# Kernel tuning notes

Measured on AMD Instinct MI355X. Metric: run time of the kernel, lower is better.

Reference implementation:

```python
import jax, jax.numpy as jnp
import numpy as np

INF = 100000.0
B, W, T, U, S, N = 64, 16, 64, 128, 20, 8


def setup_inputs() -> dict:
    key = jax.random.key(0)
    ks = jax.random.split(key, 9)
    xavier = (2.0 / (U + U)) ** 0.5
    return {
        "slot_utt_h": jax.random.normal(ks[0], (B, W, T, U), jnp.float32),
        "slot_candidate_c": jax.random.normal(ks[1], (S, U), jnp.float32),
        "status_candidate_c": jax.random.normal(ks[2], (N, U), jnp.float32),
        "position_encoding": jax.random.normal(ks[3], (B, W, S, U), jnp.float32),
        "q_status": jax.random.normal(ks[4], (B, W, N, U), jnp.float32),
        "mask": jnp.zeros((B, W, S * N), jnp.float32),
        "weight": jax.random.normal(ks[5], (U, U), jnp.float32) * xavier,  # bilinear co-attention weight [U,U]
        "W1": jax.random.normal(ks[6], (2 * U, U), jnp.float32) * 0.05,
        "b1": jnp.zeros((U,), jnp.float32),
        "W2": jax.random.normal(ks[7], (U, U), jnp.float32) * 0.05,
        "b2": jnp.zeros((U,), jnp.float32),
        "W3": jax.random.normal(ks[8], (U, 1), jnp.float32) * 0.05,
        "b3": jnp.zeros((1,), jnp.float32),
    }


def _zero_mask(p):
    # original: -(p == 0).float() * INF, added before softmax
    return jnp.where(p == 0.0, -INF, 0.0)


def reference(slot_utt_h, slot_candidate_c, status_candidate_c, position_encoding,
              q_status, mask, weight, W1, b1, W2, b2, W3, b3):
    # ---- attention over utterance tokens ----
    # p[b,w,s,t] = <slot_candidate_c[s], slot_utt_h[b,w,t]>
    p = jnp.einsum('su,bwtu->bwst', slot_candidate_c, slot_utt_h)
    p = jax.nn.softmax(p + _zero_mask(p), axis=-1)
    q_slot = jnp.einsum('bwst,bwtu->bwsu', p, slot_utt_h) + position_encoding  # [B,W,S,U]

    # ---- bilinear co-attention: [B,W*S,U] @ weight @ [B,U,W*N] -> [B,W,S,W,N] ----
    co = jnp.einsum('bwsu,uv,bxnv->bwsxn', q_slot, weight, q_status)
    p2 = jax.nn.softmax(co + _zero_mask(co), axis=3)  # softmax over the second window axis x

    # weighted sum of statuses over window axis x
    q_status_slot = jnp.einsum('bwsxn,bxnu->bwsnu', p2, q_status)  # [B,W,S,N,U]

    q_slot_exp = jnp.broadcast_to(q_slot[:, :, :, None, :], (B, W, S, N, U))
    features = jnp.concatenate([q_slot_exp, q_status_slot], axis=-1)  # [B,W,S,N,2U]

    # ---- MLP (dropout in eval mode = identity) ----
    h = jax.nn.relu(features @ W1 + b1)
    h = jax.nn.relu(h @ W2 + b2)
    logits = h @ W3 + b3  # [B,W,S,N,1]

    logits = logits.reshape(B, W, S * N)
    slot_pred_logits = jnp.max(logits + mask, axis=1)  # masked max-pool over window
    slot_pred_labels = (slot_pred_logits > 0.0).astype(jnp.float32)
    return (slot_pred_labels, S * N, slot_pred_logits)
```

## Files before the change

### kernel.cpp

```cpp
#include <hip/hip_runtime.h>
#include <math.h>

#define INF_ 100000.0f
constexpr int B_ = 64, W_ = 16, T_ = 64, U_ = 128, S_ = 20, N_ = 8;

typedef unsigned short ushort_t;
typedef __attribute__((ext_vector_type(8))) short bf16x8;
typedef __attribute__((ext_vector_type(4))) float floatx4;

static __device__ __forceinline__ unsigned short f2bf(float x) {
    unsigned int u = __float_as_uint(x);
    return (unsigned short)((u + 0x7fff + ((u >> 16) & 1)) >> 16);
}
static __device__ __forceinline__ float bf2f(unsigned short s) {
    return __uint_as_float(((unsigned int)s) << 16);
}

__global__ __launch_bounds__(256) void k0_cast(
    const float* __restrict__ q_status, const float* __restrict__ weight,
    const float* __restrict__ W1, const float* __restrict__ W2,
    const float* __restrict__ c,
    ushort_t* __restrict__ qstat_bf, ushort_t* __restrict__ w1topT,
    ushort_t* __restrict__ w1botT, ushort_t* __restrict__ w2T,
    ushort_t* __restrict__ c_bf, ushort_t* __restrict__ Gt_bf)
{
    __shared__ __align__(16) ushort_t sw[128 * 136];
    __shared__ __align__(16) ushort_t sq[128 * 136];

    const int tid = threadIdx.x;

    if (blockIdx.x < 1076) {
        int g = blockIdx.x * 256 + tid;
        if (g < 262144) {
            int i = g * 4;
            float4 v = *(const float4*)&q_status[i];
            ushort4 o = {f2bf(v.x), f2bf(v.y), f2bf(v.z), f2bf(v.w)};
            *(ushort4*)&qstat_bf[i] = o;
            return;
        }
        g -= 262144;
        if (g < 4096) {
            int i = g * 4, j = i >> 7, k = i & 127;
            ushort4 o = {f2bf(W1[k * 128 + j]), f2bf(W1[(k + 1) * 128 + j]),
                         f2bf(W1[(k + 2) * 128 + j]), f2bf(W1[(k + 3) * 128 + j])};
            *(ushort4*)&w1topT[i] = o;
            return;
        }
        g -= 4096;
        if (g < 4096) {
            int i = g * 4, j = i >> 7, k = i & 127;
            ushort4 o = {f2bf(W1[(128 + k) * 128 + j]), f2bf(W1[(129 + k) * 128 + j]),
                         f2bf(W1[(130 + k) * 128 + j]), f2bf(W1[(131 + k) * 128 + j])};
            *(ushort4*)&w1botT[i] = o;
            return;
        }
        g -= 4096;
        if (g < 4096) {
            int i = g * 4, j = i >> 7, k = i & 127;
            ushort4 o = {f2bf(W2[k * 128 + j]), f2bf(W2[(k + 1) * 128 + j]),
                         f2bf(W2[(k + 2) * 128 + j]), f2bf(W2[(k + 3) * 128 + j])};
            *(ushort4*)&w2T[i] = o;
            return;
        }
        g -= 4096;
        if (g < 1024) {
            int i = g * 4, s = i >> 7;
            ushort4 o = {0, 0, 0, 0};
            if (s < 20) {
                float4 v = *(const float4*)&c[i];
                o = (ushort4){f2bf(v.x), f2bf(v.y), f2bf(v.z), f2bf(v.w)};
            }
            *(ushort4*)&c_bf[i] = o;
            return;
        }
        return;
    }

    const int b = blockIdx.x - 1076;
    const float* qb = q_status + (size_t)b * 16384;
    for (int i = tid * 4; i < 16384; i += 1024) {
        int r = i >> 7, v = i & 127;
        float4 wv = *(const float4*)&weight[i];
        ushort4 ow = {f2bf(wv.x), f2bf(wv.y), f2bf(wv.z), f2bf(wv.w)};
        *(ushort4*)&sw[r * 136 + v] = ow;
        float4 qv = *(const float4*)&qb[i];
        ushort4 oq = {f2bf(qv.x), f2bf(qv.y), f2bf(qv.z), f2bf(qv.w)};
        *(ushort4*)&sq[r * 136 + v] = oq;
    }
    __syncthreads();

    const int wave = tid >> 6, lane = tid & 63, m16 = lane & 15, q = lane >> 4;
    ushort_t* Gb = Gt_bf + (size_t)b * 16384;
#pragma unroll
    for (int ci = 0; ci < 16; ++ci) {
        int tile = wave * 16 + ci;
        int mt = tile >> 3, jt = tile & 7;
        floatx4 acc = {0.f, 0.f, 0.f, 0.f};
#pragma unroll
        for (int kt = 0; kt < 4; ++kt) {
            bf16x8 a = *(const bf16x8*)&sq[(mt * 16 + m16) * 136 + kt * 32 + q * 8];
            bf16x8 w = *(const bf16x8*)&sw[(jt * 16 + m16) * 136 + kt * 32 + q * 8];
            acc = __builtin_amdgcn_mfma_f32_16x16x32_bf16(a, w, acc, 0, 0, 0);
        }
#pragma unroll
        for (int reg = 0; reg < 4; ++reg)
            Gb[(mt * 16 + q * 4 + reg) * 128 + jt * 16 + m16] = f2bf(acc[reg]);
    }
}

__global__ __launch_bounds__(256) void k1_attn(
    const float* __restrict__ h,
    const ushort_t* __restrict__ c_bf,
    const float* __restrict__ pos,
    ushort_t* __restrict__ q_slot_bf)
{
    __shared__ __align__(16) ushort_t sh_h[64 * 136];
    __shared__ __align__(16) ushort_t sh_hT[128 * 72];
    __shared__ __align__(16) float    sh_sc[32 * 68];
    __shared__ __align__(16) ushort_t sh_P[32 * 72];

    const int bw = blockIdx.x, tid = threadIdx.x;
    const float* hb = h + (size_t)bw * 8192;
    for (int i = tid; i < 8192; i += 256) {
        int t = i >> 7, u = i & 127;
        ushort_t v = f2bf(hb[i]);
        sh_h[t * 136 + u] = v;
        sh_hT[u * 72 + t] = v;
    }
    for (int i = tid; i < 32 * 72; i += 256) sh_P[i] = 0;
    __syncthreads();

    const int wave = tid >> 6, lane = tid & 63, m16 = lane & 15, q = lane >> 4;

#pragma unroll
    for (int ci = 0; ci < 2; ++ci) {
        int cmb = wave * 2 + ci;
        int mt = cmb >> 2, jt = cmb & 3;
        floatx4 acc = {0.f, 0.f, 0.f, 0.f};
#pragma unroll
        for (int kt = 0; kt < 4; ++kt) {
            bf16x8 a = *(const bf16x8*)&c_bf[(mt * 16 + m16) * 128 + kt * 32 + q * 8];
            bf16x8 b = *(const bf16x8*)&sh_h[(jt * 16 + m16) * 136 + kt * 32 + q * 8];
            acc = __builtin_amdgcn_mfma_f32_16x16x32_bf16(a, b, acc, 0, 0, 0);
        }
#pragma unroll
        for (int reg = 0; reg < 4; ++reg)
            sh_sc[(mt * 16 + q * 4 + reg) * 68 + jt * 16 + m16] = acc[reg];
    }
    __syncthreads();

    for (int s = wave; s < 20; s += 4) {
        float v = sh_sc[s * 68 + lane];
        if (v == 0.0f) v = -INF_;
        float m = v;
        for (int d = 32; d; d >>= 1) m = fmaxf(m, __shfl_xor(m, d));
        float e = expf(v - m);
        float sum = e;
        for (int d = 32; d; d >>= 1) sum += __shfl_xor(sum, d);
        sh_P[s * 72 + lane] = f2bf(e / sum);
    }
    __syncthreads();

    const size_t obase = (size_t)bw * 2560;
#pragma unroll
    for (int ci = 0; ci < 4; ++ci) {
        int cmb = wave * 4 + ci;
        int mt = cmb >> 3, jt = cmb & 7;
        floatx4 acc = {0.f, 0.f, 0.f, 0.f};
#pragma unroll
        for (int kt = 0; kt < 2; ++kt) {
            bf16x8 a = *(const bf16x8*)&sh_P[(mt * 16 + m16) * 72 + kt * 32 + q * 8];
            bf16x8 b = *(const bf16x8*)&sh_hT[(jt * 16 + m16) * 72 + kt * 32 + q * 8];
            acc = __builtin_amdgcn_mfma_f32_16x16x32_bf16(a, b, acc, 0, 0, 0);
        }
        int u = jt * 16 + m16;
#pragma unroll
        for (int reg = 0; reg < 4; ++reg) {
            int row = mt * 16 + q * 4 + reg;
            if (row < 20)
                q_slot_bf[obase + row * 128 + u] =
                    f2bf(acc[reg] + pos[obase + row * 128 + u]);
        }
    }
}

__global__ __launch_bounds__(512, 2) void k2ab(
    const ushort_t* __restrict__ qs_bf,
    const ushort_t* __restrict__ w1topT,
    const float* __restrict__ b1,
    const ushort_t* __restrict__ qstat_bf,
    const ushort_t* __restrict__ w1botT,
    float* __restrict__ A,
    ushort_t* __restrict__ qs1T_bf)
{
    __shared__ __align__(16) ushort_t sh_w[128 * 136];
    const int tid = threadIdx.x;
    const int wave = tid >> 6, lane = tid & 63, m16 = lane & 15, q = lane >> 4;

    if (blockIdx.x < 160) {
        for (int i = tid * 4; i < 16384; i += 2048) {
            int j = i >> 7, k = i & 127;
            *(ushort4*)&sh_w[j * 136 + k] = *(const ushort4*)&w1topT[i];
        }
        __syncthreads();

        const size_t row = (size_t)blockIdx.x * 128 + wave * 16 + m16;
        floatx4 acc[8];
#pragma unroll
        for (int jt = 0; jt < 8; ++jt) acc[jt] = (floatx4){0.f, 0.f, 0.f, 0.f};
#pragma unroll
        for (int kt = 0; kt < 4; ++kt) {
            bf16x8 a = *(const bf16x8*)&qs_bf[row * 128 + kt * 32 + q * 8];
#pragma unroll
            for (int jt = 0; jt < 8; ++jt) {
                bf16x8 b = *(const bf16x8*)&sh_w[(jt * 16 + m16) * 136 + kt * 32 + q * 8];
                acc[jt] = __builtin_amdgcn_mfma_f32_16x16x32_bf16(a, b, acc[jt], 0, 0, 0);
            }
        }
        const size_t orow0 = (size_t)blockIdx.x * 128 + wave * 16 + q * 4;
#pragma unroll
        for (int jt = 0; jt < 8; ++jt) {
            int col = jt * 16 + m16;
            float bv = b1[col];
#pragma unroll
            for (int reg = 0; reg < 4; ++reg)
                A[(orow0 + reg) * 128 + col] = acc[jt][reg] + bv;
        }
    } else {
        const int blk = blockIdx.x - 160;
        for (int i = tid * 4; i < 16384; i += 2048) {
            int j = i >> 7, k = i & 127;
            *(ushort4*)&sh_w[j * 136 + k] = *(const ushort4*)&w1botT[i];
        }
        __syncthreads();

        const size_t row = (size_t)blk * 128 + wave * 16 + m16;
        floatx4 acc[8];
#pragma unroll
        for (int jt = 0; jt < 8; ++jt) acc[jt] = (floatx4){0.f, 0.f, 0.f, 0.f};
#pragma unroll
        for (int kt = 0; kt < 4; ++kt) {
            bf16x8 a = *(const bf16x8*)&qstat_bf[row * 128 + kt * 32 + q * 8];
#pragma unroll
            for (int jt = 0; jt < 8; ++jt) {
                bf16x8 b = *(const bf16x8*)&sh_w[(jt * 16 + m16) * 136 + kt * 32 + q * 8];
                acc[jt] = __builtin_amdgcn_mfma_f32_16x16x32_bf16(a, b, acc[jt], 0, 0, 0);
            }
        }
        const size_t orow0 = (size_t)blk * 128 + wave * 16 + q * 4;
#pragma unroll
        for (int jt = 0; jt < 8; ++jt) {
            int col = jt * 16 + m16;
#pragma unroll
            for (int reg = 0; reg < 4; ++reg) {
                size_t grow = orow0 + reg;
                qs1T_bf[(grow >> 7) * 16384 + (size_t)col * 128 + (grow & 127)]
                    = f2bf(acc[jt][reg]);
            }
        }
    }
}

__global__ __launch_bounds__(640, 5) void k4_fused(
    const ushort_t* __restrict__ q_slot_bf,
    const ushort_t* __restrict__ Gt_bf,
    const ushort_t* __restrict__ qs1T_bf,
    const float* __restrict__ A,
    const ushort_t* __restrict__ w2T,
    const float* __restrict__ b2,
    const float* __restrict__ W3,
    const float* __restrict__ b3,
    float* __restrict__ lg)
{
    __shared__ __align__(16) ushort_t sh_w2t[128 * 136];
    __shared__ __align__(16) ushort_t sh_u[22688];

    const int bw = blockIdx.x, b = bw >> 4, tid = threadIdx.x;

    for (int i = tid * 4; i < 16384; i += 2560) {
        int r = i >> 7, k = i & 127;
        *(ushort4*)&sh_w2t[r * 136 + k] = *(const ushort4*)&w2T[i];
        *(ushort4*)&sh_u[r * 136 + k] =
            *(const ushort4*)&Gt_bf[(size_t)b * 16384 + i];
    }
    __syncthreads();

    const int wave = tid >> 6, lane = tid & 63, m16 = lane & 15, q = lane >> 4;

    if (wave < 8) {
        const ushort_t* qsl = q_slot_bf + (size_t)bw * 2560;
        const bf16x8 zz = {0, 0, 0, 0, 0, 0, 0, 0};
#pragma unroll
        for (int ci = 0; ci < 2; ++ci) {
            int tile = wave * 2 + ci;
            int mt = tile >> 3, jt = tile & 7;
            int arow = mt * 16 + m16;
            floatx4 acc = {0.f, 0.f, 0.f, 0.f};
#pragma unroll
            for (int kt = 0; kt < 4; ++kt) {
                bf16x8 a = (arow < 20)
                    ? *(const bf16x8*)&qsl[arow * 128 + kt * 32 + q * 8] : zz;
                bf16x8 g = *(const bf16x8*)&sh_u[(jt * 16 + m16) * 136 + kt * 32 + q * 8];
                acc = __builtin_amdgcn_mfma_f32_16x16x32_bf16(a, g, acc, 0, 0, 0);
            }
#pragma unroll
            for (int reg = 0; reg < 4; ++reg) {
                int row = mt * 16 + q * 4 + reg;
                if (row < 20)
                    sh_u[20048 + row * 132 + jt * 16 + m16] = f2bf(acc[reg]);
            }
        }
    }
    __syncthreads();

    {
        ushort4 rq[7];
#pragma unroll 7
        for (int jj = 0; jj < 7; ++jj) {
            int i = tid * 4 + jj * 2560;
            if (i < 16384)
                rq[jj] = *(const ushort4*)&qs1T_bf[(size_t)b * 16384 + i];
        }

        int sn = tid >> 2, xi = tid & 3;
        int s = sn >> 3, n = sn & 7;
        const ushort_t* crow = &sh_u[20048 + s * 132];
        float v[4];
        float m = -INFINITY;
#pragma unroll
        for (int j = 0; j < 4; ++j) {
            float t = bf2f(crow[(xi + 4 * j) * 8 + n]);
            if (t == 0.0f) t = -INF_;
            v[j] = t;
            m = fmaxf(m, t);
        }
        m = fmaxf(m, __shfl_xor(m, 1));
        m = fmaxf(m, __shfl_xor(m, 2));
        float sum = 0.f;
#pragma unroll
        for (int j = 0; j < 4; ++j) { v[j] = expf(v[j] - m); sum += v[j]; }
        sum += __shfl_xor(sum, 1);
        sum += __shfl_xor(sum, 2);
        float r = 1.0f / sum;
#pragma unroll
        for (int j = 0; j < 4; ++j)
            sh_u[17408 + s * 132 + (xi + 4 * j) * 8 + n] = f2bf(v[j] * r);

#pragma unroll 7
        for (int jj = 0; jj < 7; ++jj) {
            int i = tid * 4 + jj * 2560;
            if (i < 16384) {
                int r2 = i >> 7, k2 = i & 127;
                *(ushort4*)&sh_u[r2 * 136 + k2] = rq[jj];
            }
        }
    }
    __syncthreads();

    const int n = m16 & 7;
    const int sIdx = wave * 2 + (m16 >> 3);
    const int rowS = wave * 16 + m16;

    floatx4 gacc[8];
#pragma unroll
    for (int mt = 0; mt < 8; ++mt) gacc[mt] = (floatx4){0.f, 0.f, 0.f, 0.f};

#pragma unroll
    for (int kt = 0; kt < 4; ++kt) {
        short pv = (short)sh_u[17408 + sIdx * 132 + kt * 32 + q * 8 + n];
        bf16x8 pf = {0, 0, 0, 0, 0, 0, 0, 0};
        pf[0] = (n == 0) ? pv : (short)0;
        pf[1] = (n == 1) ? pv : (short)0;
        pf[2] = (n == 2) ? pv : (short)0;
        pf[3] = (n == 3) ? pv : (short)0;
        pf[4] = (n == 4) ? pv : (short)0;
        pf[5] = (n == 5) ? pv : (short)0;
        pf[6] = (n == 6) ? pv : (short)0;
        pf[7] = (n == 7) ? pv : (short)0;
#pragma unroll
        for (int mt = 0; mt < 8; ++mt) {
            bf16x8 af = *(const bf16x8*)&sh_u[(mt * 16 + m16) * 136 + kt * 32 + q * 8];
            gacc[mt] = __builtin_amdgcn_mfma_f32_16x16x32_bf16(af, pf, gacc[mt], 0, 0, 0);
        }
    }
    __syncthreads();

    {
        const float* Ab = A + ((size_t)bw * 20 + sIdx) * 128;
#pragma unroll
        for (int mt = 0; mt < 8; ++mt) {
            int u0 = mt * 16 + q * 4;
            float4 av = *(const float4*)&Ab[u0];
            ushort4 o;
            o.x = f2bf(fmaxf(gacc[mt][0] + av.x, 0.f));
            o.y = f2bf(fmaxf(gacc[mt][1] + av.y, 0.f));
            o.z = f2bf(fmaxf(gacc[mt][2] + av.z, 0.f));
            o.w = f2bf(fmaxf(gacc[mt][3] + av.w, 0.f));
            *(ushort4*)&sh_u[rowS * 136 + u0] = o;
        }
    }
    __syncthreads();

    floatx4 acc[8];
#pragma unroll
    for (int jt = 0; jt < 8; ++jt) acc[jt] = (floatx4){0.f, 0.f, 0.f, 0.f};

#pragma unroll
    for (int kt = 0; kt < 4; ++kt) {
        const int k0 = kt * 32 + q * 8;
        bf16x8 af = *(const bf16x8*)&sh_u[rowS * 136 + k0];
#pragma unroll
        for (int jt = 0; jt < 8; ++jt) {
            bf16x8 bfr = *(const bf16x8*)&sh_w2t[(jt * 16 + m16) * 136 + k0];
            acc[jt] = __builtin_amdgcn_mfma_f32_16x16x32_bf16(af, bfr, acc[jt], 0, 0, 0);
        }
    }

    float b2v[8], w3v[8];
#pragma unroll
    for (int jt = 0; jt < 8; ++jt) {
        b2v[jt] = b2[jt * 16 + m16];
        w3v[jt] = W3[jt * 16 + m16];
    }
    const float b3v = b3[0];

#pragma unroll
    for (int reg = 0; reg < 4; ++reg) {
        float p = 0.f;
#pragma unroll
        for (int jt = 0; jt < 8; ++jt)
            p += fmaxf(acc[jt][reg] + b2v[jt], 0.f) * w3v[jt];
        p += __shfl_xor(p, 1);
        p += __shfl_xor(p, 2);
        p += __shfl_xor(p, 4);
        p += __shfl_xor(p, 8);
        if (m16 == 0)
            lg[(size_t)bw * 160 + wave * 16 + q * 4 + reg] = p + b3v;
    }
}

__global__ __launch_bounds__(256) void k5_final(
    const float* __restrict__ lg,
    const float* __restrict__ mask,
    float* __restrict__ out)
{
    int idx = blockIdx.x * 256 + threadIdx.x;
    const int SN = S_ * N_;
    if (idx < B_ * SN) {
        int b = idx / SN, sn = idx % SN;
        float m = -INFINITY;
        for (int w = 0; w < W_; ++w) {
            float v = lg[((size_t)b * W_ + w) * SN + sn] + mask[((size_t)b * W_ + w) * SN + sn];
            m = fmaxf(m, v);
        }
        out[idx] = (m > 0.f) ? 1.f : 0.f;
        out[B_ * SN + 1 + idx] = m;
    }
    if (idx == 0) out[B_ * SN] = (float)SN;
}

extern "C" void kernel_launch(void* const* d_in, const int* in_sizes, int n_in,
                              void* d_out, int out_size, void* d_ws, size_t ws_size,
                              hipStream_t stream) {
    const float* slot_utt_h = (const float*)d_in[0];
    const float* slot_candidate_c = (const float*)d_in[1];
    const float* position_encoding = (const float*)d_in[3];
    const float* q_status = (const float*)d_in[4];
    const float* mask = (const float*)d_in[5];
    const float* weight = (const float*)d_in[6];
    const float* W1 = (const float*)d_in[7];
    const float* b1 = (const float*)d_in[8];
    const float* W2 = (const float*)d_in[9];
    const float* b2 = (const float*)d_in[10];
    const float* W3 = (const float*)d_in[11];
    const float* b3 = (const float*)d_in[12];
    float* out = (float*)d_out;

    float* f = (float*)d_ws;
    ushort_t* q_slot_bf = (ushort_t*)(f + 0);
    float*    A         = f + 1310720;
    ushort_t* qs1T_bf   = (ushort_t*)(f + 3932160);
    ushort_t* Gt_bf     = (ushort_t*)(f + 4456448);
    ushort_t* qstat_bf  = (ushort_t*)(f + 4980736);
    float*    lg        = f + 5505024;
    ushort_t* w1topT    = (ushort_t*)(f + 5668864);
    ushort_t* w1botT    = (ushort_t*)(f + 5677056);
    ushort_t* w2T       = (ushort_t*)(f + 5685248);
    ushort_t* c_bf      = (ushort_t*)(f + 5693440);

    k0_cast<<<1140, 256, 0, stream>>>(q_status, weight, W1, W2,
                                      slot_candidate_c,
                                      qstat_bf, w1topT, w1botT, w2T, c_bf, Gt_bf);
    k1_attn<<<1024, 256, 0, stream>>>(slot_utt_h, c_bf,
                                      position_encoding, q_slot_bf);
    k2ab<<<224, 512, 0, stream>>>(q_slot_bf, w1topT, b1, qstat_bf, w1botT,
                                  A, qs1T_bf);
    k4_fused<<<1024, 640, 0, stream>>>(q_slot_bf, Gt_bf, qs1T_bf, A, w2T,
                                       b2, W3, b3, lg);
    k5_final<<<(B_ * S_ * N_ + 255) / 256, 256, 0, stream>>>(lg, mask, out);
}
```

Baseline: 181.6 us.

## Fuse attention, co-attention and MLP into one per-window kernel

```diff
diff --git a/kernel.cpp b/kernel.cpp
--- a/kernel.cpp
+++ b/kernel.cpp
@@ -16,315 +16,246 @@
     return __uint_as_float(((unsigned int)s) << 16);
 }
 
-__global__ __launch_bounds__(256) void k0_cast(
+__global__ __launch_bounds__(256) void k_pre(
     const float* __restrict__ q_status, const float* __restrict__ weight,
     const float* __restrict__ W1, const float* __restrict__ W2,
     const float* __restrict__ c,
-    ushort_t* __restrict__ qstat_bf, ushort_t* __restrict__ w1topT,
-    ushort_t* __restrict__ w1botT, ushort_t* __restrict__ w2T,
-    ushort_t* __restrict__ c_bf, ushort_t* __restrict__ Gt_bf)
+    ushort_t* __restrict__ w1topT, ushort_t* __restrict__ w2T,
+    ushort_t* __restrict__ c_bf,
+    ushort_t* __restrict__ Gt_bf, ushort_t* __restrict__ qs1T_bf)
 {
     __shared__ __align__(16) ushort_t sw[128 * 136];
     __shared__ __align__(16) ushort_t sq[128 * 136];
-
-    const int tid = threadIdx.x;
-
-    if (blockIdx.x < 1076) {
-        int g = blockIdx.x * 256 + tid;
-        if (g < 262144) {
-            int i = g * 4;
-            float4 v = *(const float4*)&q_status[i];
-            ushort4 o = {f2bf(v.x), f2bf(v.y), f2bf(v.z), f2bf(v.w)};
-            *(ushort4*)&qstat_bf[i] = o;
-            return;
-        }
-        g -= 262144;
-        if (g < 4096) {
-            int i = g * 4, j = i >> 7, k = i & 127;
-            ushort4 o = {f2bf(W1[k * 128 + j]), f2bf(W1[(k + 1) * 128 + j]),
-                         f2bf(W1[(k + 2) * 128 + j]), f2bf(W1[(k + 3) * 128 + j])};
-            *(ushort4*)&w1topT[i] = o;
-            return;
-        }
-        g -= 4096;
-        if (g < 4096) {
-            int i = g * 4, j = i >> 7, k = i & 127;
-            ushort4 o = {f2bf(W1[(128 + k) * 128 + j]), f2bf(W1[(129 + k) * 128 + j]),
-                         f2bf(W1[(130 + k) * 128 + j]), f2bf(W1[(131 + k) * 128 + j])};
-            *(ushort4*)&w1botT[i] = o;
-            return;
-        }
-        g -= 4096;
-        if (g < 4096) {
-            int i = g * 4, j = i >> 7, k = i & 127;
-            ushort4 o = {f2bf(W2[k * 128 + j]), f2bf(W2[(k + 1) * 128 + j]),
-                         f2bf(W2[(k + 2) * 128 + j]), f2bf(W2[(k + 3) * 128 + j])};
-            *(ushort4*)&w2T[i] = o;
-            return;
-        }
-        g -= 4096;
-        if (g < 1024) {
-            int i = g * 4, s = i >> 7;
-            ushort4 o = {0, 0, 0, 0};
-            if (s < 20) {
-                float4 v = *(const float4*)&c[i];
-                o = (ushort4){f2bf(v.x), f2bf(v.y), f2bf(v.z), f2bf(v.w)};
-            }
-            *(ushort4*)&c_bf[i] = o;
-            return;
+    const int tid = threadIdx.x, bx = blockIdx.x;
+
+    if (bx < 64) {
+        const int b = bx;
+        const float* qb = q_status + (size_t)b * 16384;
+        for (int i = tid * 4; i < 16384; i += 1024) {
+            int r = i >> 7, v = i & 127;
+            float4 wv = *(const float4*)&weight[i];
+            *(ushort4*)&sw[r * 136 + v] =
+                (ushort4){f2bf(wv.x), f2bf(wv.y), f2bf(wv.z), f2bf(wv.w)};
+            float4 qv = *(const float4*)&qb[i];
+            *(ushort4*)&sq[r * 136 + v] =
+                (ushort4){f2bf(qv.x), f2bf(qv.y), f2bf(qv.z), f2bf(qv.w)};
+        }
+        __syncthreads();
+        const int wave = tid >> 6, lane = tid & 63, m16 = lane & 15, q = lane >> 4;
+        ushort_t* Gb = Gt_bf + (size_t)b * 16384;
+#pragma unroll
+        for (int ci = 0; ci < 16; ++ci) {
+            int tile = wave * 16 + ci;
+            int mt = tile >> 3, jt = tile & 7;
+            floatx4 acc = {0.f, 0.f, 0.f, 0.f};
+#pragma unroll
+            for (int kt = 0; kt < 4; ++kt) {
+                bf16x8 a = *(const bf16x8*)&sq[(mt * 16 + m16) * 136 + kt * 32 + q * 8];
+                bf16x8 w = *(const bf16x8*)&sw[(jt * 16 + m16) * 136 + kt * 32 + q * 8];
+                acc = __builtin_amdgcn_mfma_f32_16x16x32_bf16(a, w, acc, 0, 0, 0);
+            }
+#pragma unroll
+            for (int reg = 0; reg < 4; ++reg)
+                Gb[(mt * 16 + q * 4 + reg) * 128 + jt * 16 + m16] = f2bf(acc[reg]);
         }
         return;
     }
-
-    const int b = blockIdx.x - 1076;
-    const float* qb = q_status + (size_t)b * 16384;
-    for (int i = tid * 4; i < 16384; i += 1024) {
-        int r = i >> 7, v = i & 127;
-        float4 wv = *(const float4*)&weight[i];
-        ushort4 ow = {f2bf(wv.x), f2bf(wv.y), f2bf(wv.z), f2bf(wv.w)};
-        *(ushort4*)&sw[r * 136 + v] = ow;
-        float4 qv = *(const float4*)&qb[i];
-        ushort4 oq = {f2bf(qv.x), f2bf(qv.y), f2bf(qv.z), f2bf(qv.w)};
-        *(ushort4*)&sq[r * 136 + v] = oq;
-    }
-    __syncthreads();
-
-    const int wave = tid >> 6, lane = tid & 63, m16 = lane & 15, q = lane >> 4;
-    ushort_t* Gb = Gt_bf + (size_t)b * 16384;
-#pragma unroll
-    for (int ci = 0; ci < 16; ++ci) {
-        int tile = wave * 16 + ci;
-        int mt = tile >> 3, jt = tile & 7;
-        floatx4 acc = {0.f, 0.f, 0.f, 0.f};
-#pragma unroll
-        for (int kt = 0; kt < 4; ++kt) {
-            bf16x8 a = *(const bf16x8*)&sq[(mt * 16 + m16) * 136 + kt * 32 + q * 8];
-            bf16x8 w = *(const bf16x8*)&sw[(jt * 16 + m16) * 136 + kt * 32 + q * 8];
-            acc = __builtin_amdgcn_mfma_f32_16x16x32_bf16(a, w, acc, 0, 0, 0);
-        }
-#pragma unroll
-        for (int reg = 0; reg < 4; ++reg)
-            Gb[(mt * 16 + q * 4 + reg) * 128 + jt * 16 + m16] = f2bf(acc[reg]);
-    }
-}
-
-__global__ __launch_bounds__(256) void k1_attn(
+    if (bx < 128) {
+        const int b = bx - 64;
+        const float* qb = q_status + (size_t)b * 16384;
+        for (int i = tid * 4; i < 16384; i += 1024) {
+            int r = i >> 7, v = i & 127;
+            float4 qv = *(const float4*)&qb[i];
+            *(ushort4*)&sq[r * 136 + v] =
+                (ushort4){f2bf(qv.x), f2bf(qv.y), f2bf(qv.z), f2bf(qv.w)};
+            int v2 = i >> 7, j = i & 127;
+            float4 wv = *(const float4*)&W1[(128 + v2) * 128 + j];
+            sw[(j + 0) * 136 + v2] = f2bf(wv.x);
+            sw[(j + 1) * 136 + v2] = f2bf(wv.y);
+            sw[(j + 2) * 136 + v2] = f2bf(wv.z);
+            sw[(j + 3) * 136 + v2] = f2bf(wv.w);
+        }
+        __syncthreads();
+        const int wave = tid >> 6, lane = tid & 63, m16 = lane & 15, q = lane >> 4;
+        ushort_t* Qb = qs1T_bf + (size_t)b * 16384;
+#pragma unroll
+        for (int ci = 0; ci < 16; ++ci) {
+            int tile = wave * 16 + ci;
+            int mt = tile >> 3, jt = tile & 7;
+            floatx4 acc = {0.f, 0.f, 0.f, 0.f};
+#pragma unroll
+            for (int kt = 0; kt < 4; ++kt) {
+                bf16x8 a = *(const bf16x8*)&sq[(mt * 16 + m16) * 136 + kt * 32 + q * 8];
+                bf16x8 w = *(const bf16x8*)&sw[(jt * 16 + m16) * 136 + kt * 32 + q * 8];
+                acc = __builtin_amdgcn_mfma_f32_16x16x32_bf16(a, w, acc, 0, 0, 0);
+            }
+            ushort4 o = {f2bf(acc[0]), f2bf(acc[1]), f2bf(acc[2]), f2bf(acc[3])};
+            *(ushort4*)&Qb[(jt * 16 + m16) * 128 + mt * 16 + q * 4] = o;
+        }
+        return;
+    }
+    if (bx < 144) {
+        int g = (bx - 128) * 1024 + tid * 4;
+        int j = g >> 7, k = g & 127;
+        *(ushort4*)&w1topT[g] =
+            (ushort4){f2bf(W1[k * 128 + j]), f2bf(W1[(k + 1) * 128 + j]),
+                      f2bf(W1[(k + 2) * 128 + j]), f2bf(W1[(k + 3) * 128 + j])};
+        return;
+    }
+    if (bx < 160) {
+        int g = (bx - 144) * 1024 + tid * 4;
+        int j = g >> 7, k = g & 127;
+        *(ushort4*)&w2T[g] =
+            (ushort4){f2bf(W2[k * 128 + j]), f2bf(W2[(k + 1) * 128 + j]),
+                      f2bf(W2[(k + 2) * 128 + j]), f2bf(W2[(k + 3) * 128 + j])};
+        return;
+    }
+    for (int i = tid * 4; i < 4096; i += 1024) {
+        int s = i >> 7;
+        ushort4 o = {0, 0, 0, 0};
+        if (s < 20) {
+            float4 v = *(const float4*)&c[i];
+            o = (ushort4){f2bf(v.x), f2bf(v.y), f2bf(v.z), f2bf(v.w)};
+        }
+        *(ushort4*)&c_bf[i] = o;
+    }
+}
+
+__global__ __launch_bounds__(640, 5) void k_main(
     const float* __restrict__ h,
     const ushort_t* __restrict__ c_bf,
     const float* __restrict__ pos,
-    ushort_t* __restrict__ q_slot_bf)
-{
-    __shared__ __align__(16) ushort_t sh_h[64 * 136];
-    __shared__ __align__(16) ushort_t sh_hT[128 * 72];
-    __shared__ __align__(16) float    sh_sc[32 * 68];
-    __shared__ __align__(16) ushort_t sh_P[32 * 72];
-
-    const int bw = blockIdx.x, tid = threadIdx.x;
-    const float* hb = h + (size_t)bw * 8192;
-    for (int i = tid; i < 8192; i += 256) {
-        int t = i >> 7, u = i & 127;
-        ushort_t v = f2bf(hb[i]);
-        sh_h[t * 136 + u] = v;
-        sh_hT[u * 72 + t] = v;
-    }
-    for (int i = tid; i < 32 * 72; i += 256) sh_P[i] = 0;
-    __syncthreads();
-
-    const int wave = tid >> 6, lane = tid & 63, m16 = lane & 15, q = lane >> 4;
-
-#pragma unroll
-    for (int ci = 0; ci < 2; ++ci) {
-        int cmb = wave * 2 + ci;
-        int mt = cmb >> 2, jt = cmb & 3;
-        floatx4 acc = {0.f, 0.f, 0.f, 0.f};
-#pragma unroll
-        for (int kt = 0; kt < 4; ++kt) {
-            bf16x8 a = *(const bf16x8*)&c_bf[(mt * 16 + m16) * 128 + kt * 32 + q * 8];
-            bf16x8 b = *(const bf16x8*)&sh_h[(jt * 16 + m16) * 136 + kt * 32 + q * 8];
-            acc = __builtin_amdgcn_mfma_f32_16x16x32_bf16(a, b, acc, 0, 0, 0);
-        }
-#pragma unroll
-        for (int reg = 0; reg < 4; ++reg)
-            sh_sc[(mt * 16 + q * 4 + reg) * 68 + jt * 16 + m16] = acc[reg];
-    }
-    __syncthreads();
-
-    for (int s = wave; s < 20; s += 4) {
-        float v = sh_sc[s * 68 + lane];
-        if (v == 0.0f) v = -INF_;
-        float m = v;
-        for (int d = 32; d; d >>= 1) m = fmaxf(m, __shfl_xor(m, d));
-        float e = expf(v - m);
-        float sum = e;
-        for (int d = 32; d; d >>= 1) sum += __shfl_xor(sum, d);
-        sh_P[s * 72 + lane] = f2bf(e / sum);
-    }
-    __syncthreads();
-
-    const size_t obase = (size_t)bw * 2560;
-#pragma unroll
-    for (int ci = 0; ci < 4; ++ci) {
-        int cmb = wave * 4 + ci;
-        int mt = cmb >> 3, jt = cmb & 7;
-        floatx4 acc = {0.f, 0.f, 0.f, 0.f};
-#pragma unroll
-        for (int kt = 0; kt < 2; ++kt) {
-            bf16x8 a = *(const bf16x8*)&sh_P[(mt * 16 + m16) * 72 + kt * 32 + q * 8];
-            bf16x8 b = *(const bf16x8*)&sh_hT[(jt * 16 + m16) * 72 + kt * 32 + q * 8];
-            acc = __builtin_amdgcn_mfma_f32_16x16x32_bf16(a, b, acc, 0, 0, 0);
-        }
-        int u = jt * 16 + m16;
-#pragma unroll
-        for (int reg = 0; reg < 4; ++reg) {
-            int row = mt * 16 + q * 4 + reg;
-            if (row < 20)
-                q_slot_bf[obase + row * 128 + u] =
-                    f2bf(acc[reg] + pos[obase + row * 128 + u]);
-        }
-    }
-}
-
-__global__ __launch_bounds__(512, 2) void k2ab(
-    const ushort_t* __restrict__ qs_bf,
+    const ushort_t* __restrict__ Gt_bf,
+    const ushort_t* __restrict__ qs1T_bf,
     const ushort_t* __restrict__ w1topT,
     const float* __restrict__ b1,
-    const ushort_t* __restrict__ qstat_bf,
-    const ushort_t* __restrict__ w1botT,
-    float* __restrict__ A,
-    ushort_t* __restrict__ qs1T_bf)
-{
-    __shared__ __align__(16) ushort_t sh_w[128 * 136];
-    const int tid = threadIdx.x;
-    const int wave = tid >> 6, lane = tid & 63, m16 = lane & 15, q = lane >> 4;
-
-    if (blockIdx.x < 160) {
-        for (int i = tid * 4; i < 16384; i += 2048) {
-            int j = i >> 7, k = i & 127;
-            *(ushort4*)&sh_w[j * 136 + k] = *(const ushort4*)&w1topT[i];
-        }
-        __syncthreads();
-
-        const size_t row = (size_t)blockIdx.x * 128 + wave * 16 + m16;
-        floatx4 acc[8];
-#pragma unroll
-        for (int jt = 0; jt < 8; ++jt) acc[jt] = (floatx4){0.f, 0.f, 0.f, 0.f};
-#pragma unroll
-        for (int kt = 0; kt < 4; ++kt) {
-            bf16x8 a = *(const bf16x8*)&qs_bf[row * 128 + kt * 32 + q * 8];
-#pragma unroll
-            for (int jt = 0; jt < 8; ++jt) {
-                bf16x8 b = *(const bf16x8*)&sh_w[(jt * 16 + m16) * 136 + kt * 32 + q * 8];
-                acc[jt] = __builtin_amdgcn_mfma_f32_16x16x32_bf16(a, b, acc[jt], 0, 0, 0);
-            }
-        }
-        const size_t orow0 = (size_t)blockIdx.x * 128 + wave * 16 + q * 4;
-#pragma unroll
-        for (int jt = 0; jt < 8; ++jt) {
-            int col = jt * 16 + m16;
-            float bv = b1[col];
-#pragma unroll
-            for (int reg = 0; reg < 4; ++reg)
-                A[(orow0 + reg) * 128 + col] = acc[jt][reg] + bv;
-        }
-    } else {
-        const int blk = blockIdx.x - 160;
-        for (int i = tid * 4; i < 16384; i += 2048) {
-            int j = i >> 7, k = i & 127;
-            *(ushort4*)&sh_w[j * 136 + k] = *(const ushort4*)&w1botT[i];
-        }
-        __syncthreads();
-
-        const size_t row = (size_t)blk * 128 + wave * 16 + m16;
-        floatx4 acc[8];
-#pragma unroll
-        for (int jt = 0; jt < 8; ++jt) acc[jt] = (floatx4){0.f, 0.f, 0.f, 0.f};
-#pragma unroll
-        for (int kt = 0; kt < 4; ++kt) {
-            bf16x8 a = *(const bf16x8*)&qstat_bf[row * 128 + kt * 32 + q * 8];
-#pragma unroll
-            for (int jt = 0; jt < 8; ++jt) {
-                bf16x8 b = *(const bf16x8*)&sh_w[(jt * 16 + m16) * 136 + kt * 32 + q * 8];
-                acc[jt] = __builtin_amdgcn_mfma_f32_16x16x32_bf16(a, b, acc[jt], 0, 0, 0);
-            }
-        }
-        const size_t orow0 = (size_t)blk * 128 + wave * 16 + q * 4;
-#pragma unroll
-        for (int jt = 0; jt < 8; ++jt) {
-            int col = jt * 16 + m16;
-#pragma unroll
-            for (int reg = 0; reg < 4; ++reg) {
-                size_t grow = orow0 + reg;
-                qs1T_bf[(grow >> 7) * 16384 + (size_t)col * 128 + (grow & 127)]
-                    = f2bf(acc[jt][reg]);
-            }
-        }
-    }
-}
-
-__global__ __launch_bounds__(640, 5) void k4_fused(
-    const ushort_t* __restrict__ q_slot_bf,
-    const ushort_t* __restrict__ Gt_bf,
-    const ushort_t* __restrict__ qs1T_bf,
-    const float* __restrict__ A,
     const ushort_t* __restrict__ w2T,
     const float* __restrict__ b2,
     const float* __restrict__ W3,
     const float* __restrict__ b3,
     float* __restrict__ lg)
 {
-    __shared__ __align__(16) ushort_t sh_w2t[128 * 136];
-    __shared__ __align__(16) ushort_t sh_u[22688];
+    __shared__ __align__(16) ushort_t sh[39168];
 
     const int bw = blockIdx.x, b = bw >> 4, tid = threadIdx.x;
-
-    for (int i = tid * 4; i < 16384; i += 2560) {
-        int r = i >> 7, k = i & 127;
-        *(ushort4*)&sh_w2t[r * 136 + k] = *(const ushort4*)&w2T[i];
-        *(ushort4*)&sh_u[r * 136 + k] =
-            *(const ushort4*)&Gt_bf[(size_t)b * 16384 + i];
-    }
-    __syncthreads();
-
     const int wave = tid >> 6, lane = tid & 63, m16 = lane & 15, q = lane >> 4;
 
+    const float* hb = h + (size_t)bw * 8192;
+    for (int i = tid * 4; i < 8192; i += 2560) {
+        int t = i >> 7, u = i & 127;
+        float4 v = *(const float4*)&hb[i];
+        ushort4 o = {f2bf(v.x), f2bf(v.y), f2bf(v.z), f2bf(v.w)};
+        *(ushort4*)&sh[t * 136 + u] = o;
+        sh[8704 + (u + 0) * 72 + t] = o.x;
+        sh[8704 + (u + 1) * 72 + t] = o.y;
+        sh[8704 + (u + 2) * 72 + t] = o.z;
+        sh[8704 + (u + 3) * 72 + t] = o.w;
+    }
+    for (int i = tid; i < 2304; i += 640) sh[22272 + i] = 0;
+    __syncthreads();
+
+    {
+        float* sc = (float*)sh + 8960;
+        if (wave < 8) {
+            int mt = wave >> 2, jt = wave & 3;
+            floatx4 acc = {0.f, 0.f, 0.f, 0.f};
+#pragma unroll
+            for (int kt = 0; kt < 4; ++kt) {
+                bf16x8 a = *(const bf16x8*)&c_bf[(mt * 16 + m16) * 128 + kt * 32 + q * 8];
+                bf16x8 bb = *(const bf16x8*)&sh[(jt * 16 + m16) * 136 + kt * 32 + q * 8];
+                acc = __builtin_amdgcn_mfma_f32_16x16x32_bf16(a, bb, acc, 0, 0, 0);
+            }
+#pragma unroll
+            for (int reg = 0; reg < 4; ++reg)
+                sc[(mt * 16 + q * 4 + reg) * 68 + jt * 16 + m16] = acc[reg];
+        }
+    }
+    __syncthreads();
+
+    {
+        const float* sc = (const float*)sh + 8960;
+        for (int s = wave; s < 20; s += 10) {
+            float v = sc[s * 68 + lane];
+            if (v == 0.0f) v = -INF_;
+            float m = v;
+            for (int d = 32; d; d >>= 1) m = fmaxf(m, __shfl_xor(m, d));
+            float e = expf(v - m);
+            float sum = e;
+            for (int d = 32; d; d >>= 1) sum += __shfl_xor(sum, d);
+            sh[22272 + s * 72 + lane] = f2bf(e / sum);
+        }
+    }
+    __syncthreads();
+
     if (wave < 8) {
-        const ushort_t* qsl = q_slot_bf + (size_t)bw * 2560;
-        const bf16x8 zz = {0, 0, 0, 0, 0, 0, 0, 0};
+        const size_t obase = (size_t)bw * 2560;
 #pragma unroll
         for (int ci = 0; ci < 2; ++ci) {
-            int tile = wave * 2 + ci;
-            int mt = tile >> 3, jt = tile & 7;
-            int arow = mt * 16 + m16;
+            int cmb = wave * 2 + ci;
+            int mt = cmb >> 3, jt = cmb & 7;
             floatx4 acc = {0.f, 0.f, 0.f, 0.f};
 #pragma unroll
-            for (int kt = 0; kt < 4; ++kt) {
-                bf16x8 a = (arow < 20)
-                    ? *(const bf16x8*)&qsl[arow * 128 + kt * 32 + q * 8] : zz;
-                bf16x8 g = *(const bf16x8*)&sh_u[(jt * 16 + m16) * 136 + kt * 32 + q * 8];
-                acc = __builtin_amdgcn_mfma_f32_16x16x32_bf16(a, g, acc, 0, 0, 0);
-            }
+            for (int kt = 0; kt < 2; ++kt) {
+                bf16x8 a = *(const bf16x8*)&sh[22272 + (mt * 16 + m16) * 72 + kt * 32 + q * 8];
+                bf16x8 bb = *(const bf16x8*)&sh[8704 + (jt * 16 + m16) * 72 + kt * 32 + q * 8];
+                acc = __builtin_amdgcn_mfma_f32_16x16x32_bf16(a, bb, acc, 0, 0, 0);
+            }
+            int u = jt * 16 + m16;
 #pragma unroll
             for (int reg = 0; reg < 4; ++reg) {
                 int row = mt * 16 + q * 4 + reg;
                 if (row < 20)
-                    sh_u[20048 + row * 132 + jt * 16 + m16] = f2bf(acc[reg]);
-            }
-        }
-    }
-    __syncthreads();
-
+                    sh[17920 + row * 136 + u] =
+                        f2bf(acc[reg] + pos[obase + row * 128 + u]);
+            }
+        }
+    }
+    __syncthreads();
+
+    for (int i = tid * 4; i < 16384; i += 2560) {
+        int r = i >> 7, k2 = i & 127;
+        *(ushort4*)&sh[r * 136 + k2] = *(const ushort4*)&qs1T_bf[(size_t)b * 16384 + i];
+    }
     {
-        ushort4 rq[7];
-#pragma unroll 7
-        for (int jj = 0; jj < 7; ++jj) {
-            int i = tid * 4 + jj * 2560;
-            if (i < 16384)
-                rq[jj] = *(const ushort4*)&qs1T_bf[(size_t)b * 16384 + i];
-        }
-
+        const bf16x8 zz = {0, 0, 0, 0, 0, 0, 0, 0};
+        float* Af = (float*)sh + 13776;
+        const ushort_t* Gb = Gt_bf + (size_t)b * 16384;
+        for (int t = wave; t < 32; t += 10) {
+            int isA = t >> 4, tt = t & 15;
+            int mt = tt >> 3, jt = tt & 7;
+            int arow = mt * 16 + m16;
+            const ushort_t* Bsrc = isA ? w1topT : Gb;
+            floatx4 acc = {0.f, 0.f, 0.f, 0.f};
+#pragma unroll
+            for (int kt = 0; kt < 4; ++kt) {
+                bf16x8 a = (arow < 20)
+                    ? *(const bf16x8*)&sh[17920 + arow * 136 + kt * 32 + q * 8] : zz;
+                bf16x8 g = *(const bf16x8*)&Bsrc[(jt * 16 + m16) * 128 + kt * 32 + q * 8];
+                acc = __builtin_amdgcn_mfma_f32_16x16x32_bf16(a, g, acc, 0, 0, 0);
+            }
+            int col = jt * 16 + m16;
+            if (isA) {
+                float bv = b1[col];
+#pragma unroll
+                for (int reg = 0; reg < 4; ++reg) {
+                    int row = mt * 16 + q * 4 + reg;
+                    if (row < 20) Af[row * 132 + col] = acc[reg] + bv;
+                }
+            } else {
+#pragma unroll
+                for (int reg = 0; reg < 4; ++reg) {
+                    int row = mt * 16 + q * 4 + reg;
+                    if (row < 20) sh[22272 + row * 132 + col] = f2bf(acc[reg]);
+                }
+            }
+        }
+    }
+    __syncthreads();
+
+    {
         int sn = tid >> 2, xi = tid & 3;
         int s = sn >> 3, n = sn & 7;
-        const ushort_t* crow = &sh_u[20048 + s * 132];
+        const ushort_t* crow = &sh[22272 + s * 132];
         float v[4];
         float m = -INFINITY;
 #pragma unroll
@@ -344,16 +275,7 @@
         float r = 1.0f / sum;
 #pragma unroll
         for (int j = 0; j < 4; ++j)
-            sh_u[17408 + s * 132 + (xi + 4 * j) * 8 + n] = f2bf(v[j] * r);
-
-#pragma unroll 7
-        for (int jj = 0; jj < 7; ++jj) {
-            int i = tid * 4 + jj * 2560;
-            if (i < 16384) {
-                int r2 = i >> 7, k2 = i & 127;
-                *(ushort4*)&sh_u[r2 * 136 + k2] = rq[jj];
-            }
-        }
+            sh[24912 + s * 132 + (xi + 4 * j) * 8 + n] = f2bf(v[j] * r);
     }
     __syncthreads();
 
@@ -364,10 +286,9 @@
     floatx4 gacc[8];
 #pragma unroll
     for (int mt = 0; mt < 8; ++mt) gacc[mt] = (floatx4){0.f, 0.f, 0.f, 0.f};
-
 #pragma unroll
     for (int kt = 0; kt < 4; ++kt) {
-        short pv = (short)sh_u[17408 + sIdx * 132 + kt * 32 + q * 8 + n];
+        short pv = (short)sh[24912 + sIdx * 132 + kt * 32 + q * 8 + n];
         bf16x8 pf = {0, 0, 0, 0, 0, 0, 0, 0};
         pf[0] = (n == 0) ? pv : (short)0;
         pf[1] = (n == 1) ? pv : (short)0;
@@ -379,39 +300,44 @@
         pf[7] = (n == 7) ? pv : (short)0;
 #pragma unroll
         for (int mt = 0; mt < 8; ++mt) {
-            bf16x8 af = *(const bf16x8*)&sh_u[(mt * 16 + m16) * 136 + kt * 32 + q * 8];
+            bf16x8 af = *(const bf16x8*)&sh[(mt * 16 + m16) * 136 + kt * 32 + q * 8];
             gacc[mt] = __builtin_amdgcn_mfma_f32_16x16x32_bf16(af, pf, gacc[mt], 0, 0, 0);
         }
     }
     __syncthreads();
 
     {
-        const float* Ab = A + ((size_t)bw * 20 + sIdx) * 128;
+        const float* Af = (const float*)sh + 13776 + sIdx * 132;
 #pragma unroll
         for (int mt = 0; mt < 8; ++mt) {
             int u0 = mt * 16 + q * 4;
-            float4 av = *(const float4*)&Ab[u0];
+            float4 av = *(const float4*)&Af[u0];
             ushort4 o;
             o.x = f2bf(fmaxf(gacc[mt][0] + av.x, 0.f));
             o.y = f2bf(fmaxf(gacc[mt][1] + av.y, 0.f));
             o.z = f2bf(fmaxf(gacc[mt][2] + av.z, 0.f));
             o.w = f2bf(fmaxf(gacc[mt][3] + av.w, 0.f));
-            *(ushort4*)&sh_u[rowS * 136 + u0] = o;
-        }
+            *(ushort4*)&sh[rowS * 136 + u0] = o;
+        }
+    }
+    __syncthreads();
+
+    for (int i = tid * 4; i < 16384; i += 2560) {
+        int r = i >> 7, k2 = i & 127;
+        *(ushort4*)&sh[21760 + r * 136 + k2] = *(const ushort4*)&w2T[i];
     }
     __syncthreads();
 
     floatx4 acc[8];
 #pragma unroll
     for (int jt = 0; jt < 8; ++jt) acc[jt] = (floatx4){0.f, 0.f, 0.f, 0.f};
-
 #pragma unroll
     for (int kt = 0; kt < 4; ++kt) {
         const int k0 = kt * 32 + q * 8;
-        bf16x8 af = *(const bf16x8*)&sh_u[rowS * 136 + k0];
+        bf16x8 af = *(const bf16x8*)&sh[rowS * 136 + k0];
 #pragma unroll
         for (int jt = 0; jt < 8; ++jt) {
-            bf16x8 bfr = *(const bf16x8*)&sh_w2t[(jt * 16 + m16) * 136 + k0];
+            bf16x8 bfr = *(const bf16x8*)&sh[21760 + (jt * 16 + m16) * 136 + k0];
             acc[jt] = __builtin_amdgcn_mfma_f32_16x16x32_bf16(af, bfr, acc[jt], 0, 0, 0);
         }
     }
@@ -477,25 +403,18 @@
     float* out = (float*)d_out;
 
     float* f = (float*)d_ws;
-    ushort_t* q_slot_bf = (ushort_t*)(f + 0);
-    float*    A         = f + 1310720;
-    ushort_t* qs1T_bf   = (ushort_t*)(f + 3932160);
-    ushort_t* Gt_bf     = (ushort_t*)(f + 4456448);
-    ushort_t* qstat_bf  = (ushort_t*)(f + 4980736);
-    float*    lg        = f + 5505024;
-    ushort_t* w1topT    = (ushort_t*)(f + 5668864);
-    ushort_t* w1botT    = (ushort_t*)(f + 5677056);
-    ushort_t* w2T       = (ushort_t*)(f + 5685248);
-    ushort_t* c_bf      = (ushort_t*)(f + 5693440);
-
-    k0_cast<<<1140, 256, 0, stream>>>(q_status, weight, W1, W2,
-                                      slot_candidate_c,
-                                      qstat_bf, w1topT, w1botT, w2T, c_bf, Gt_bf);
-    k1_attn<<<1024, 256, 0, stream>>>(slot_utt_h, c_bf,
-                                      position_encoding, q_slot_bf);
-    k2ab<<<224, 512, 0, stream>>>(q_slot_bf, w1topT, b1, qstat_bf, w1botT,
-                                  A, qs1T_bf);
-    k4_fused<<<1024, 640, 0, stream>>>(q_slot_bf, Gt_bf, qs1T_bf, A, w2T,
-                                       b2, W3, b3, lg);
+    float*    lg       = f + 0;
+    ushort_t* Gt_bf    = (ushort_t*)(f + 163840);
+    ushort_t* qs1T_bf  = (ushort_t*)(f + 688128);
+    ushort_t* w1topT   = (ushort_t*)(f + 1212416);
+    ushort_t* w2T      = (ushort_t*)(f + 1220608);
+    ushort_t* c_bf     = (ushort_t*)(f + 1228800);
+
+    k_pre<<<161, 256, 0, stream>>>(q_status, weight, W1, W2,
+                                   slot_candidate_c,
+                                   w1topT, w2T, c_bf, Gt_bf, qs1T_bf);
+    k_main<<<1024, 640, 0, stream>>>(slot_utt_h, c_bf, position_encoding,
+                                     Gt_bf, qs1T_bf, w1topT, b1, w2T,
+                                     b2, W3, b3, lg);
     k5_final<<<(B_ * S_ * N_ + 255) / 256, 256, 0, stream>>>(lg, mask, out);
 }
```

New measurement: 187.8 us. 1.03x slower.
